# Performance work log

Measured on AMD Instinct MI355X. Metric: run time of the kernel, lower is better.

Reference implementation:

```python
import jax, jax.numpy as jnp
import numpy as np

B, CIN, COUT, K, NS, NIN, H = 4, 128, 128, 9, 16384, 16384, 64
W0 = 30.0  # SIREN first-layer frequency


def setup_inputs() -> dict:
    ks = jax.random.split(jax.random.key(0), 8)
    x = jax.random.normal(ks[0], (B, CIN, NIN), dtype=jnp.float32)
    neighbours = jax.random.randint(ks[1], (K, NS), 0, NIN)
    # normalized relative neighbour coordinates in [-1, 1], shape (K*NS, 2)
    coords = 2.0 * jax.random.uniform(ks[2], (K * NS, 2), dtype=jnp.float32) - 1.0
    W1 = jax.random.normal(ks[3], (2, H), dtype=jnp.float32) / jnp.sqrt(2.0)
    b1 = jnp.zeros((H,), dtype=jnp.float32)
    W2 = jax.random.normal(ks[4], (H, H), dtype=jnp.float32) / jnp.sqrt(H * 1.0)
    b2 = jnp.zeros((H,), dtype=jnp.float32)
    W3 = jax.random.normal(ks[5], (H, COUT * CIN), dtype=jnp.float32) / jnp.sqrt(H * 1.0)
    b3 = jnp.zeros((COUT * CIN,), dtype=jnp.float32)
    bias = jnp.zeros((1, COUT, 1), dtype=jnp.float32)
    return {"x": x, "neighbours": neighbours, "coords": coords,
            "W1": W1, "b1": b1, "W2": W2, "b2": b2, "W3": W3, "b3": b3,
            "bias": bias}


def reference(x, neighbours, coords, W1, b1, W2, b2, W3, b3, bias):
    k, ns = neighbours.shape
    cin = x.shape[1]
    cout = W3.shape[1] // cin
    # INR filter generation: (K*NS, 2) -> (K*NS, COUT*CIN)
    h = jnp.sin(W0 * (coords @ W1 + b1))
    h = jnp.sin(h @ W2 + b2)
    f = h @ W3 + b3                                  # (K*NS, COUT*CIN)
    # (K*NS, COUT, CIN) -> (COUT, CIN, K, NS), matching torch permute(1,2,0).reshape
    f = f.reshape(k * ns, cout, cin).transpose(1, 2, 0).reshape(cout, cin, k, ns)
    # neighbor gather: (B, CIN, K, NS)
    x_unfold = x[:, :, neighbours]
    # weighted reduce over (CIN, K) per output location
    out = jnp.einsum('bjkl,ijkl->bil', x_unfold, f)
    return out + bias
```

## Files before the change

kernel.cpp:

```cpp
#include <hip/hip_runtime.h>

#define NS   16384
#define NIN  16384
#define CIN  128
#define COUT 128
#define KNB  9
#define MCH  66
#define QDIM (CIN*MCH)
#define W0C  30.0f

typedef __bf16 bf16;
typedef bf16  bf16x8  __attribute__((ext_vector_type(8)));
typedef float floatx4 __attribute__((ext_vector_type(4)));
typedef unsigned int u32;

__device__ inline unsigned short f2bf(float f){
  u32 u = __float_as_uint(f);
  u += 0x7fffu + ((u >> 16) & 1u);
  return (unsigned short)(u >> 16);
}
__device__ inline u32 pack2bf(float lo, float hi){
  return (u32)f2bf(lo) | ((u32)f2bf(hi) << 16);
}
__device__ inline float bf2f(unsigned short s){
  return __uint_as_float((u32)s << 16);
}

__global__ void k0_vt(const float* __restrict__ W3, const float* __restrict__ b3,
                      unsigned short* __restrict__ Vt){
  int idx = blockIdx.x*256 + threadIdx.x;
  if (idx >= COUT*QDIM) return;
  int i = idx / QDIM;
  int q = idx - i*QDIM;
  int m = q >> 7;
  int j = q & 127;
  float v = 0.f;
  if (m < 64)       v = W3[m*16384 + i*128 + j];
  else if (m == 64) v = b3[i*128 + j];
  Vt[idx] = f2bf(v);
}

__global__ __launch_bounds__(256) void k1_mlp(const float* __restrict__ coords,
      const float* __restrict__ W1, const float* __restrict__ b1,
      const float* __restrict__ W2, const float* __restrict__ b2,
      unsigned short* __restrict__ h){
  int lane = threadIdx.x & 63;
  int pt = blockIdx.x*4 + (threadIdx.x >> 6);
  float c0 = coords[2*pt], c1 = coords[2*pt+1];
  float z  = fmaf(c0, W1[lane], fmaf(c1, W1[64+lane], b1[lane]));
  float h1 = sinf(W0C * z);
  float acc = b2[lane];
  #pragma unroll
  for (int mp = 0; mp < 64; ++mp)
    acc = fmaf(__shfl(h1, mp, 64), W2[mp*64 + lane], acc);
  float h2 = sinf(acc);
  size_t base = (size_t)pt * MCH;
  h[base + lane] = f2bf(h2);
  if (lane == 0){ h[base+64] = 0x3F80; h[base+65] = 0; }
}

__global__ __launch_bounds__(256) void k1tp(const unsigned short* __restrict__ h,
                                            u32* __restrict__ hTp){
  __shared__ unsigned short t[128][68];
  int pt0 = blockIdx.x*128;
  int tid = threadIdx.x;
  for (int e = tid; e < 128*MCH; e += 256){
    int p = e / MCH, m = e - p*MCH;
    t[p][m] = h[(size_t)(pt0 + p)*MCH + m];
  }
  __syncthreads();
  for (int e = tid; e < 33*128; e += 256){
    int g = e >> 7, p = e & 127;
    hTp[(size_t)g*(KNB*NS) + pt0 + p] = (u32)t[p][2*g] | ((u32)t[p][2*g+1] << 16);
  }
}

__global__ void k_tr(const float* __restrict__ x, unsigned short* __restrict__ xT){
  __shared__ __align__(16) float t[32][33];
  int b  = blockIdx.z;
  int j0 = blockIdx.y*32;
  int p0 = blockIdx.x*32;
  int tx = threadIdx.x, ty = threadIdx.y;
  const float*    xb  = x  + (size_t)b*CIN*NIN;
  unsigned short* xTb = xT + (size_t)b*NIN*CIN;
  #pragma unroll
  for (int n = 0; n < 4; ++n)
    t[ty+8*n][tx] = xb[(size_t)(j0+ty+8*n)*NIN + p0+tx];
  __syncthreads();
  #pragma unroll
  for (int n = 0; n < 4; ++n)
    xTb[(size_t)(p0+ty+8*n)*CIN + j0+tx] = f2bf(t[tx][ty+8*n]);
}

__global__ __launch_bounds__(512, 4) void k_fused(
      const unsigned short* __restrict__ xT,
      const u32* __restrict__ hTp,
      const int* __restrict__ nb,
      const unsigned short* __restrict__ Vt,
      const float* __restrict__ bias,
      float* __restrict__ out){
  __shared__ __align__(16) unsigned short A[2][32][136];
  __shared__ u32 hm2[KNB][32];
  __shared__ int pk[KNB][32];

  const int tid = threadIdx.x;
  const int r0  = blockIdx.x * 32;
  const int b   = r0 >> 14;
  const int l0  = r0 & (NS-1);

  if (tid < KNB*32){
    int k = tid >> 5, l = tid & 31;
    pk[k][l] = nb[k*NS + l0 + l];
  }
  __syncthreads();

  const int lq = tid >> 4;
  const int jc = tid & 15;
  const char* xbB = (const char*)(xT + ((size_t)b << 21));
  bf16x8 xk[KNB];
  #pragma unroll
  for (int k = 0; k < KNB; ++k)
    xk[k] = *(const bf16x8*)(xbB + (((size_t)(u32)pk[k][lq]) << 8) + (size_t)jc*16);

  const int lane  = tid & 63;
  const int w     = tid >> 6;
  const int ar    = lane & 15;
  const int klane = lane >> 4;

  floatx4 acc[2];
  acc[0] = (floatx4){0.f,0.f,0.f,0.f};
  acc[1] = (floatx4){0.f,0.f,0.f,0.f};

  const char* VtB = (const char*)Vt + (size_t)(w*16 + ar)*(QDIM*2) + (size_t)klane*16;

  for (int mg = 0; mg < 33; ++mg){
    if (tid < KNB*32){
      int k = tid >> 5, l = tid & 31;
      hm2[k][l] = hTp[(size_t)mg*(KNB*NS) + ((size_t)k << 14) + l0 + l];
    }
    __syncthreads();

    float a2x[8], a2y[8];
    #pragma unroll
    for (int t = 0; t < 8; ++t){ a2x[t] = 0.f; a2y[t] = 0.f; }
    #pragma unroll
    for (int k = 0; k < KNB; ++k){
      u32 hw = hm2[k][lq];
      float hk0 = bf2f((unsigned short)(hw & 0xffff));
      float hk1 = bf2f((unsigned short)(hw >> 16));
      #pragma unroll
      for (int t = 0; t < 8; ++t){
        float xf = (float)xk[k][t];
        a2x[t] = fmaf(xf, hk0, a2x[t]);
        a2y[t] = fmaf(xf, hk1, a2y[t]);
      }
    }
    {
      u32 p0[4], p1[4];
      #pragma unroll
      for (int t = 0; t < 4; ++t){
        p0[t] = pack2bf(a2x[2*t], a2x[2*t+1]);
        p1[t] = pack2bf(a2y[2*t], a2y[2*t+1]);
      }
      *(uint4*)&A[0][lq][jc*8] = *(uint4*)p0;
      *(uint4*)&A[1][lq][jc*8] = *(uint4*)p1;
    }
    __syncthreads();

    #pragma unroll
    for (int mm = 0; mm < 2; ++mm){
      const char* Ab = (const char*)&A[mm][0][0] + (size_t)klane*16;
      const char* Vg = VtB + (size_t)((mg*2 + mm)*128)*2;
      #pragma unroll
      for (int kt = 0; kt < 4; ++kt){
        bf16x8 bv = *(const bf16x8*)(Vg + kt*64);
        bf16x8 av0 = *(const bf16x8*)(Ab + (0*16 + ar)*272 + kt*64);
        bf16x8 av1 = *(const bf16x8*)(Ab + (1*16 + ar)*272 + kt*64);
        acc[0] = __builtin_amdgcn_mfma_f32_16x16x32_bf16(av0, bv, acc[0], 0, 0, 0);
        acc[1] = __builtin_amdgcn_mfma_f32_16x16x32_bf16(av1, bv, acc[1], 0, 0, 0);
      }
    }
    __syncthreads();
  }

  float* ob = out + ((size_t)b << 21);
  int i = w*16 + ar;
  float bi = bias[i];
  #pragma unroll
  for (int rf = 0; rf < 2; ++rf){
    int l = l0 + rf*16 + klane*4;
    float4 v;
    v.x = acc[rf][0] + bi;
    v.y = acc[rf][1] + bi;
    v.z = acc[rf][2] + bi;
    v.w = acc[rf][3] + bi;
    *(float4*)(ob + ((size_t)i << 14) + l) = v;
  }
}

__global__ __launch_bounds__(256) void k_naive(const float* __restrict__ x,
      const int* __restrict__ nb, const float* __restrict__ coords,
      const float* __restrict__ W1, const float* __restrict__ b1,
      const float* __restrict__ W2, const float* __restrict__ b2,
      const float* __restrict__ W3, const float* __restrict__ b3,
      const float* __restrict__ bias, float* __restrict__ out){
  __shared__ __align__(16) float hk[KNB][68];
  __shared__ int pk[KNB];
  __shared__ __align__(16) float xg[4][KNB][128];
  __shared__ __align__(16) float ul[128][66];
  int tid = threadIdx.x;
  int l = blockIdx.x;
  int lane = tid & 63, wid = tid >> 6;
  if (tid < KNB) pk[tid] = nb[tid*NS + l];
  for (int k = wid; k < KNB; k += 4){
    int pt = k*NS + l;
    float c0 = coords[2*pt], c1 = coords[2*pt+1];
    float z  = fmaf(c0, W1[lane], fmaf(c1, W1[64+lane], b1[lane]));
    float h1 = sinf(W0C*z);
    float a = b2[lane];
    for (int mp = 0; mp < 64; ++mp)
      a = fmaf(__shfl(h1, mp, 64), W2[mp*64+lane], a);
    hk[k][lane] = sinf(a);
    if (lane == 0){ hk[k][64] = 1.f; hk[k][65] = 0.f; }
  }
  __syncthreads();
  for (int idx = tid; idx < 4*KNB*128; idx += 256){
    int b = idx / (KNB*128);
    int r = idx - b*KNB*128;
    int k = r >> 7;
    int j = r & 127;
    xg[b][k][j] = x[((size_t)b*CIN + j)*NIN + pk[k]];
  }
  __syncthreads();
  for (int b = 0; b < 4; ++b){
    for (int idx = tid; idx < 128*65; idx += 256){
      int j = idx / 65, m = idx - j*65;
      float s = 0.f;
      for (int k = 0; k < KNB; ++k) s = fmaf(xg[b][k][j], hk[k][m], s);
      ul[j][m] = s;
    }
    __syncthreads();
    if (tid < 128){
      int i = tid;
      float v = bias[i];
      for (int j = 0; j < 128; ++j){
        const float* wcol = W3 + i*128 + j;
        for (int m = 0; m < 64; ++m)
          v = fmaf(ul[j][m], wcol[(size_t)m*16384], v);
        v = fmaf(ul[j][64], b3[i*128+j], v);
      }
      out[((size_t)b<<21) + ((size_t)i<<14) + l] = v;
    }
    __syncthreads();
  }
}

extern "C" void kernel_launch(void* const* d_in, const int* in_sizes, int n_in,
                              void* d_out, int out_size, void* d_ws, size_t ws_size,
                              hipStream_t stream) {
  const float* x      = (const float*)d_in[0];
  const int*   nb     = (const int*)  d_in[1];
  const float* coords = (const float*)d_in[2];
  const float* W1     = (const float*)d_in[3];
  const float* b1     = (const float*)d_in[4];
  const float* W2     = (const float*)d_in[5];
  const float* b2     = (const float*)d_in[6];
  const float* W3     = (const float*)d_in[7];
  const float* b3     = (const float*)d_in[8];
  const float* bias   = (const float*)d_in[9];
  float* out = (float*)d_out;

  const size_t VT_BYTES = (size_t)COUT*QDIM*2;
  const size_t H_BYTES  = (size_t)KNB*NS*MCH*2;
  const size_t HT_BYTES = (size_t)33*KNB*NS*4;
  const size_t XT_BYTES = (size_t)4*NIN*CIN*2;
  const size_t FIXED    = VT_BYTES + H_BYTES + HT_BYTES + XT_BYTES;

  if (ws_size >= FIXED) {
    char* ws = (char*)d_ws;
    unsigned short* Vt = (unsigned short*)ws;
    unsigned short* h  = (unsigned short*)(ws + VT_BYTES);
    u32*            hTp= (u32*)(ws + VT_BYTES + H_BYTES);
    unsigned short* xT = (unsigned short*)(ws + VT_BYTES + H_BYTES + HT_BYTES);

    k0_vt<<<(COUT*QDIM + 255)/256, 256, 0, stream>>>(W3, b3, Vt);
    k1_mlp<<<(KNB*NS)/4, 256, 0, stream>>>(coords, W1, b1, W2, b2, h);
    k1tp<<<(KNB*NS)/128, 256, 0, stream>>>(h, hTp);
    k_tr<<<dim3(NIN/32, CIN/32, 4), dim3(32, 8), 0, stream>>>(x, xT);
    k_fused<<<(4*NS)/32, 512, 0, stream>>>(xT, hTp, nb, Vt, bias, out);
  } else {
    k_naive<<<NS, 256, 0, stream>>>(x, nb, coords, W1, b1, W2, b2, W3, b3, bias, out);
  }
  (void)in_sizes; (void)n_in; (void)out_size;
}
```

Before: 731.8 us.

## Pair neighbours for bf16 dot2, double-buffer LDS, prefetch V and h into registers

The h intermediate is re-laid out so neighbour pairs (k, k+1) are packed per channel. This lets the per-iteration contraction over K use bf16 dot2 instructions on packed x pairs instead of scalar FMAs. The fused loop now double-buffers the A tile and the h slice in LDS, which drops one barrier per iteration. It also prefetches the next Vt fragments and upcoming h values into registers, and uses hardware packed bf16 conversion. The workspace aliases xT onto the h buffer once h has been repacked, which shrinks the footprint but relies on stream ordering. The extra registers held for prefetch may reduce occupancy.

```diff
diff --git a/kernel.cpp b/kernel.cpp
--- a/kernel.cpp
+++ b/kernel.cpp
@@ -11,23 +11,51 @@
 
 typedef __bf16 bf16;
 typedef bf16  bf16x8  __attribute__((ext_vector_type(8)));
+typedef bf16  bf16x2  __attribute__((ext_vector_type(2)));
+typedef unsigned short u16;
+typedef u16   u16x8   __attribute__((ext_vector_type(8)));
 typedef float floatx4 __attribute__((ext_vector_type(4)));
 typedef unsigned int u32;
 
-__device__ inline unsigned short f2bf(float f){
+__device__ inline u16 f2bf(float f){
   u32 u = __float_as_uint(f);
   u += 0x7fffu + ((u >> 16) & 1u);
-  return (unsigned short)(u >> 16);
-}
-__device__ inline u32 pack2bf(float lo, float hi){
-  return (u32)f2bf(lo) | ((u32)f2bf(hi) << 16);
-}
-__device__ inline float bf2f(unsigned short s){
+  return (u16)(u >> 16);
+}
+__device__ inline float bf2f(u16 s){
   return __uint_as_float((u32)s << 16);
 }
+__device__ inline u32 cvtpk2(float lo, float hi){
+  u32 r; asm("v_cvt_pk_bf16_f32 %0, %1, %2" : "=v"(r) : "v"(lo), "v"(hi)); return r;
+}
+
+#if defined(__has_builtin)
+# if __has_builtin(__builtin_amdgcn_fdot2_f32_bf16)
+#  define HAVE_DOT2 1
+# endif
+#endif
+#ifndef HAVE_DOT2
+# define HAVE_DOT2 0
+#endif
+
+__device__ inline float dot2bf(u32 x2, u32 h2, float c){
+#if HAVE_DOT2
+  return __builtin_amdgcn_fdot2_f32_bf16(__builtin_bit_cast(bf16x2, x2),
+                                         __builtin_bit_cast(bf16x2, h2), c, false);
+#else
+  float xl = bf2f((u16)(x2 & 0xffffu)), xh = bf2f((u16)(x2 >> 16));
+  float hl = bf2f((u16)(h2 & 0xffffu)), hh = bf2f((u16)(h2 >> 16));
+  return fmaf(xh, hh, fmaf(xl, hl, c));
+#endif
+}
+
+#define WG_BARRIER() do { \
+  asm volatile("s_waitcnt lgkmcnt(0)" ::: "memory"); \
+  __builtin_amdgcn_s_barrier(); \
+} while (0)
 
 __global__ void k0_vt(const float* __restrict__ W3, const float* __restrict__ b3,
-                      unsigned short* __restrict__ Vt){
+                      u16* __restrict__ Vt){
   int idx = blockIdx.x*256 + threadIdx.x;
   if (idx >= COUT*QDIM) return;
   int i = idx / QDIM;
@@ -43,7 +71,7 @@
 __global__ __launch_bounds__(256) void k1_mlp(const float* __restrict__ coords,
       const float* __restrict__ W1, const float* __restrict__ b1,
       const float* __restrict__ W2, const float* __restrict__ b2,
-      unsigned short* __restrict__ h){
+      u16* __restrict__ h){
   int lane = threadIdx.x & 63;
   int pt = blockIdx.x*4 + (threadIdx.x >> 6);
   float c0 = coords[2*pt], c1 = coords[2*pt+1];
@@ -59,30 +87,38 @@
   if (lane == 0){ h[base+64] = 0x3F80; h[base+65] = 0; }
 }
 
-__global__ __launch_bounds__(256) void k1tp(const unsigned short* __restrict__ h,
-                                            u32* __restrict__ hTp){
-  __shared__ unsigned short t[128][68];
-  int pt0 = blockIdx.x*128;
+__global__ __launch_bounds__(256) void k1kp(const u16* __restrict__ h,
+                                            u32* __restrict__ hK){
+  __shared__ u16 t[KNB][32][66];
+  int l0 = blockIdx.x*32;
   int tid = threadIdx.x;
-  for (int e = tid; e < 128*MCH; e += 256){
-    int p = e / MCH, m = e - p*MCH;
-    t[p][m] = h[(size_t)(pt0 + p)*MCH + m];
+  for (int e = tid; e < KNB*32*66; e += 256){
+    int k = e / (32*66);
+    int r = e - k*32*66;
+    int l = r / 66;
+    int m = r - l*66;
+    t[k][l][m] = h[((size_t)(k<<14) + l0 + l)*MCH + m];
   }
   __syncthreads();
-  for (int e = tid; e < 33*128; e += 256){
-    int g = e >> 7, p = e & 127;
-    hTp[(size_t)g*(KNB*NS) + pt0 + p] = (u32)t[p][2*g] | ((u32)t[p][2*g+1] << 16);
-  }
-}
-
-__global__ void k_tr(const float* __restrict__ x, unsigned short* __restrict__ xT){
+  for (int e = tid; e < 66*5*32; e += 256){
+    int m  = e / 160;
+    int r  = e - m*160;
+    int kp = r >> 5;
+    int l  = r & 31;
+    u32 lo = t[2*kp][l][m];
+    u32 hi = (kp < 4) ? (u32)t[2*kp+1][l][m] : 0u;
+    hK[(((size_t)m*5 + kp) << 14) + l0 + l] = lo | (hi << 16);
+  }
+}
+
+__global__ void k_tr(const float* __restrict__ x, u16* __restrict__ xT){
   __shared__ __align__(16) float t[32][33];
   int b  = blockIdx.z;
   int j0 = blockIdx.y*32;
   int p0 = blockIdx.x*32;
   int tx = threadIdx.x, ty = threadIdx.y;
-  const float*    xb  = x  + (size_t)b*CIN*NIN;
-  unsigned short* xTb = xT + (size_t)b*NIN*CIN;
+  const float* xb  = x  + (size_t)b*CIN*NIN;
+  u16*         xTb = xT + (size_t)b*NIN*CIN;
   #pragma unroll
   for (int n = 0; n < 4; ++n)
     t[ty+8*n][tx] = xb[(size_t)(j0+ty+8*n)*NIN + p0+tx];
@@ -93,14 +129,14 @@
 }
 
 __global__ __launch_bounds__(512, 4) void k_fused(
-      const unsigned short* __restrict__ xT,
-      const u32* __restrict__ hTp,
+      const u16* __restrict__ xT,
+      const u32* __restrict__ hK,
       const int* __restrict__ nb,
-      const unsigned short* __restrict__ Vt,
+      const u16* __restrict__ Vt,
       const float* __restrict__ bias,
       float* __restrict__ out){
-  __shared__ __align__(16) unsigned short A[2][32][136];
-  __shared__ u32 hm2[KNB][32];
+  __shared__ __align__(16) u16 A[2][2][32][136];
+  __shared__ u32 hs[2][2][5][32];
   __shared__ int pk[KNB][32];
 
   const int tid = threadIdx.x;
@@ -112,15 +148,40 @@
     int k = tid >> 5, l = tid & 31;
     pk[k][l] = nb[k*NS + l0 + l];
   }
-  __syncthreads();
+  WG_BARRIER();
 
   const int lq = tid >> 4;
   const int jc = tid & 15;
+
+  const bool hact = tid < 320;
+  const int  hs_  = tid / 160;
+  const int  hr_  = tid - hs_*160;
+  const int  hkp_ = hr_ >> 5;
+  const int  hl_  = hr_ & 31;
+  const u32* hKp  = hK + (((size_t)(5*hs_ + hkp_)) << 14) + l0 + hl_;
+  const size_t HSTR = (size_t)10 << 14;
+  u32 hra = 0, hrb = 0;
+  if (hact){
+    u32 h0 = hKp[0];
+    hra = hKp[HSTR];
+    hrb = hKp[2*HSTR];
+    hs[0][hs_][hkp_][hl_] = h0;
+  }
+
   const char* xbB = (const char*)(xT + ((size_t)b << 21));
-  bf16x8 xk[KNB];
-  #pragma unroll
-  for (int k = 0; k < KNB; ++k)
-    xk[k] = *(const bf16x8*)(xbB + (((size_t)(u32)pk[k][lq]) << 8) + (size_t)jc*16);
+  u32 xp[5][8];
+  #pragma unroll
+  for (int kp = 0; kp < 4; ++kp){
+    u16x8 ga = *(const u16x8*)(xbB + (((size_t)(u32)pk[2*kp  ][lq]) << 8) + (size_t)jc*16);
+    u16x8 gb = *(const u16x8*)(xbB + (((size_t)(u32)pk[2*kp+1][lq]) << 8) + (size_t)jc*16);
+    #pragma unroll
+    for (int j = 0; j < 8; ++j) xp[kp][j] = (u32)ga[j] | ((u32)gb[j] << 16);
+  }
+  {
+    u16x8 ga = *(const u16x8*)(xbB + (((size_t)(u32)pk[8][lq]) << 8) + (size_t)jc*16);
+    #pragma unroll
+    for (int j = 0; j < 8; ++j) xp[4][j] = (u32)ga[j];
+  }
 
   const int lane  = tid & 63;
   const int w     = tid >> 6;
@@ -133,54 +194,71 @@
 
   const char* VtB = (const char*)Vt + (size_t)(w*16 + ar)*(QDIM*2) + (size_t)klane*16;
 
+  bf16x8 bv[8];
+  #pragma unroll
+  for (int mm = 0; mm < 2; ++mm)
+    #pragma unroll
+    for (int kt = 0; kt < 4; ++kt)
+      bv[mm*4+kt] = *(const bf16x8*)(VtB + mm*256 + kt*64);
+
+  WG_BARRIER();
+
   for (int mg = 0; mg < 33; ++mg){
-    if (tid < KNB*32){
-      int k = tid >> 5, l = tid & 31;
-      hm2[k][l] = hTp[(size_t)mg*(KNB*NS) + ((size_t)k << 14) + l0 + l];
-    }
-    __syncthreads();
-
-    float a2x[8], a2y[8];
-    #pragma unroll
-    for (int t = 0; t < 8; ++t){ a2x[t] = 0.f; a2y[t] = 0.f; }
-    #pragma unroll
-    for (int k = 0; k < KNB; ++k){
-      u32 hw = hm2[k][lq];
-      float hk0 = bf2f((unsigned short)(hw & 0xffff));
-      float hk1 = bf2f((unsigned short)(hw >> 16));
+    const int pb = mg & 1;
+
+    float a2[2][8];
+    #pragma unroll
+    for (int s = 0; s < 2; ++s)
       #pragma unroll
-      for (int t = 0; t < 8; ++t){
-        float xf = (float)xk[k][t];
-        a2x[t] = fmaf(xf, hk0, a2x[t]);
-        a2y[t] = fmaf(xf, hk1, a2y[t]);
+      for (int j = 0; j < 8; ++j) a2[s][j] = 0.f;
+    #pragma unroll
+    for (int s = 0; s < 2; ++s){
+      #pragma unroll
+      for (int kp = 0; kp < 5; ++kp){
+        u32 hp = hs[pb][s][kp][lq];
+        #pragma unroll
+        for (int j = 0; j < 8; ++j)
+          a2[s][j] = dot2bf(xp[kp][j], hp, a2[s][j]);
       }
     }
     {
-      u32 p0[4], p1[4];
-      #pragma unroll
-      for (int t = 0; t < 4; ++t){
-        p0[t] = pack2bf(a2x[2*t], a2x[2*t+1]);
-        p1[t] = pack2bf(a2y[2*t], a2y[2*t+1]);
-      }
-      *(uint4*)&A[0][lq][jc*8] = *(uint4*)p0;
-      *(uint4*)&A[1][lq][jc*8] = *(uint4*)p1;
-    }
-    __syncthreads();
+      uint4 q0, q1;
+      q0.x = cvtpk2(a2[0][0], a2[0][1]); q0.y = cvtpk2(a2[0][2], a2[0][3]);
+      q0.z = cvtpk2(a2[0][4], a2[0][5]); q0.w = cvtpk2(a2[0][6], a2[0][7]);
+      q1.x = cvtpk2(a2[1][0], a2[1][1]); q1.y = cvtpk2(a2[1][2], a2[1][3]);
+      q1.z = cvtpk2(a2[1][4], a2[1][5]); q1.w = cvtpk2(a2[1][6], a2[1][7]);
+      *(uint4*)&A[pb][0][lq][jc*8] = q0;
+      *(uint4*)&A[pb][1][lq][jc*8] = q1;
+    }
+
+    if (hact){
+      if (mg < 32) hs[pb^1][hs_][hkp_][hl_] = hra;
+      hra = hrb;
+      if (mg <= 29) hrb = hKp[(size_t)(mg+3)*HSTR];
+    }
+
+    WG_BARRIER();
 
     #pragma unroll
     for (int mm = 0; mm < 2; ++mm){
-      const char* Ab = (const char*)&A[mm][0][0] + (size_t)klane*16;
-      const char* Vg = VtB + (size_t)((mg*2 + mm)*128)*2;
+      const char* Ab = (const char*)&A[pb][mm][0][0] + (size_t)klane*16;
       #pragma unroll
       for (int kt = 0; kt < 4; ++kt){
-        bf16x8 bv = *(const bf16x8*)(Vg + kt*64);
-        bf16x8 av0 = *(const bf16x8*)(Ab + (0*16 + ar)*272 + kt*64);
-        bf16x8 av1 = *(const bf16x8*)(Ab + (1*16 + ar)*272 + kt*64);
-        acc[0] = __builtin_amdgcn_mfma_f32_16x16x32_bf16(av0, bv, acc[0], 0, 0, 0);
-        acc[1] = __builtin_amdgcn_mfma_f32_16x16x32_bf16(av1, bv, acc[1], 0, 0, 0);
+        bf16x8 av0 = *(const bf16x8*)(Ab + (     ar)*272 + kt*64);
+        bf16x8 av1 = *(const bf16x8*)(Ab + (16 + ar)*272 + kt*64);
+        acc[0] = __builtin_amdgcn_mfma_f32_16x16x32_bf16(av0, bv[mm*4+kt], acc[0], 0, 0, 0);
+        acc[1] = __builtin_amdgcn_mfma_f32_16x16x32_bf16(av1, bv[mm*4+kt], acc[1], 0, 0, 0);
       }
     }
-    __syncthreads();
+
+    if (mg < 32){
+      const char* Vg = VtB + (size_t)(mg+1)*512;
+      #pragma unroll
+      for (int mm = 0; mm < 2; ++mm)
+        #pragma unroll
+        for (int kt = 0; kt < 4; ++kt)
+          bv[mm*4+kt] = *(const bf16x8*)(Vg + mm*256 + kt*64);
+    }
   }
 
   float* ob = out + ((size_t)b << 21);
@@ -271,23 +349,22 @@
   float* out = (float*)d_out;
 
   const size_t VT_BYTES = (size_t)COUT*QDIM*2;
+  const size_t HK_BYTES = (size_t)MCH*5*NS*4;
   const size_t H_BYTES  = (size_t)KNB*NS*MCH*2;
-  const size_t HT_BYTES = (size_t)33*KNB*NS*4;
-  const size_t XT_BYTES = (size_t)4*NIN*CIN*2;
-  const size_t FIXED    = VT_BYTES + H_BYTES + HT_BYTES + XT_BYTES;
+  const size_t FIXED    = VT_BYTES + HK_BYTES + H_BYTES;
 
   if (ws_size >= FIXED) {
     char* ws = (char*)d_ws;
     unsigned short* Vt = (unsigned short*)ws;
-    unsigned short* h  = (unsigned short*)(ws + VT_BYTES);
-    u32*            hTp= (u32*)(ws + VT_BYTES + H_BYTES);
-    unsigned short* xT = (unsigned short*)(ws + VT_BYTES + H_BYTES + HT_BYTES);
+    u32*            hK = (u32*)(ws + VT_BYTES);
+    unsigned short* h  = (unsigned short*)(ws + VT_BYTES + HK_BYTES);
+    unsigned short* xT = h;
 
     k0_vt<<<(COUT*QDIM + 255)/256, 256, 0, stream>>>(W3, b3, Vt);
     k1_mlp<<<(KNB*NS)/4, 256, 0, stream>>>(coords, W1, b1, W2, b2, h);
-    k1tp<<<(KNB*NS)/128, 256, 0, stream>>>(h, hTp);
+    k1kp<<<NS/32, 256, 0, stream>>>(h, hK);
     k_tr<<<dim3(NIN/32, CIN/32, 4), dim3(32, 8), 0, stream>>>(x, xT);
-    k_fused<<<(4*NS)/32, 512, 0, stream>>>(xT, hTp, nb, Vt, bias, out);
+    k_fused<<<(4*NS)/32, 512, 0, stream>>>(xT, hK, nb, Vt, bias, out);
   } else {
     k_naive<<<NS, 256, 0, stream>>>(x, nb, coords, W1, b1, W2, b2, W3, b3, bias, out);
   }
```

New measurement: 691.6 us. 1.06x faster.
